# Performance work log

Hardware: AMD Instinct MI355X
Metric: run time of the kernel (lower is better)

The kernel has to match this reference:

```python
import jax, jax.numpy as jnp
import numpy as np

INPUT_DIM = 2048
BATCH = 8192
SCALE = 0.1


def setup_inputs() -> dict:
    key = jax.random.key(0)
    kx, kw, kb = jax.random.split(key, 3)
    x = jax.random.normal(kx, (BATCH, INPUT_DIM), dtype=jnp.float32)
    # torch Linear default init: U(-1/sqrt(fan_in), 1/sqrt(fan_in))
    bound = 1.0 / np.sqrt(INPUT_DIM)
    W = jax.random.uniform(kw, (INPUT_DIM, INPUT_DIM), minval=-bound, maxval=bound, dtype=jnp.float32)
    b = jax.random.uniform(kb, (INPUT_DIM,), minval=-bound, maxval=bound, dtype=jnp.float32)
    return {"x": x, "W": W, "b": b}


def reference(x, W, b):
    # y = fc(x); z = y * scale * scale; out = z.sum(-1)
    y = jnp.einsum('bi,oi->bo', x, W) + b  # Linear stores weight as [out, in]
    z = y * (SCALE * SCALE)
    return z.sum(axis=-1)
```

## Files before the change

kernel.cpp:

```cpp
#include <hip/hip_runtime.h>


constexpr int IN_DIM  = 2048;
constexpr int BATCH   = 8192;
constexpr float SCALE2 = 0.01f;
constexpr int DGROUPS = 8;

__global__ __launch_bounds__(512)
void colsum_partial(const float* __restrict__ W, const float* __restrict__ bias,
                    float* __restrict__ partial, float* __restrict__ bsum) {
    const int t = threadIdx.x;
    const int b = blockIdx.x;
    const int g = b >> 6;
    const int h = b & 63;
    const int lane = t & 63, w = t >> 6;

    const float4* W4 = reinterpret_cast<const float4*>(W);
    const int c4   = (h << 3) + (t & 7);
    const int rsub = t >> 3;
    const size_t base = (size_t)((g << 8) + rsub) * (IN_DIM / 4) + c4;

    float4 acc = {0.f, 0.f, 0.f, 0.f};
    #pragma unroll
    for (int k = 0; k < 4; ++k) {
        const float4 v = W4[base + (size_t)(k << 6) * (IN_DIM / 4)];
        acc.x += v.x; acc.y += v.y; acc.z += v.z; acc.w += v.w;
    }
    #pragma unroll
    for (int m = 8; m <= 32; m <<= 1) {
        acc.x += __shfl_xor(acc.x, m); acc.y += __shfl_xor(acc.y, m);
        acc.z += __shfl_xor(acc.z, m); acc.w += __shfl_xor(acc.w, m);
    }

    __shared__ float4 redA[8][8];
    if (lane < 8) redA[w][lane] = acc;
    __syncthreads();
    if (t < 8) {
        float4 s = redA[0][t];
        #pragma unroll
        for (int j = 1; j < 8; ++j) {
            const float4 v = redA[j][t];
            s.x += v.x; s.y += v.y; s.z += v.z; s.w += v.w;
        }
        reinterpret_cast<float4*>(partial)[(size_t)g * (IN_DIM / 4) + (h << 3) + t] = s;
    }

    if (b == 0) {
        __shared__ float bs_red[8];
        float s = 0.f;
        #pragma unroll
        for (int k = 0; k < 4; ++k) s += bias[t + (k << 9)];
        #pragma unroll
        for (int off = 32; off; off >>= 1) s += __shfl_down(s, off);
        if (lane == 0) bs_red[w] = s;
        __syncthreads();
        if (t == 0) {
            float tot = 0.f;
            #pragma unroll
            for (int j = 0; j < 8; ++j) tot += bs_red[j];
            bsum[0] = tot;
        }
    }
}

__global__ __launch_bounds__(512)
void reduce_matvec(const float* __restrict__ x, const float* __restrict__ partial,
                   const float* __restrict__ bsum, float* __restrict__ out) {
    __shared__ float4 wsh4[IN_DIM / 4];
    __shared__ float  bs_sh;

    const int t    = threadIdx.x;
    const int b    = blockIdx.x;
    const int lane = t & 63;
    const int w    = t >> 6;

    const float4* p4 = reinterpret_cast<const float4*>(partial);
    float4 pv[DGROUPS];
    #pragma unroll
    for (int g = 0; g < DGROUPS; ++g)
        pv[g] = p4[(size_t)g * (IN_DIM / 4) + t];

    const float4* x4 = reinterpret_cast<const float4*>(x);
    const int r0 = (b << 4) + (w << 1);
    const size_t xb = (size_t)r0 * (IN_DIM / 4);
    float4 xv[8];
    #pragma unroll
    for (int k = 0; k < 8; ++k)
        xv[k] = x4[xb + (k << 6) + lane];

    if (t == 0) bs_sh = bsum[0];

    float4 acc = pv[0];
    #pragma unroll
    for (int g = 1; g < DGROUPS; ++g) {
        acc.x += pv[g].x; acc.y += pv[g].y;
        acc.z += pv[g].z; acc.w += pv[g].w;
    }
    wsh4[t] = acc;
    __syncthreads();

    float a0 = 0.f, a1 = 0.f;
    #pragma unroll
    for (int k = 0; k < 8; ++k) {
        const int ci = (k << 6) + lane;
        const float4 wv = wsh4[ci];
        const float4 v1 = x4[xb + 512 + ci];
        a0 += xv[k].x * wv.x + xv[k].y * wv.y + xv[k].z * wv.z + xv[k].w * wv.w;
        a1 += v1.x * wv.x + v1.y * wv.y + v1.z * wv.z + v1.w * wv.w;
    }
    #pragma unroll
    for (int off = 32; off; off >>= 1) {
        a0 += __shfl_down(a0, off);
        a1 += __shfl_down(a1, off);
    }
    if (lane == 0) {
        const float bs = bs_sh;
        *reinterpret_cast<float2*>(out + r0) =
            make_float2(SCALE2 * (a0 + bs), SCALE2 * (a1 + bs));
    }
}

extern "C" void kernel_launch(void* const* d_in, const int* in_sizes, int n_in,
                              void* d_out, int out_size, void* d_ws, size_t ws_size,
                              hipStream_t stream) {
    const float* x    = (const float*)d_in[0];
    const float* W    = (const float*)d_in[1];
    const float* bias = (const float*)d_in[2];
    float* out = (float*)d_out;
    char*  ws  = (char*)d_ws;

    float* partial = (float*)ws;
    float* bsum    = (float*)(ws + (size_t)DGROUPS * IN_DIM * sizeof(float));

    colsum_partial<<<512, 512, 0, stream>>>(W, bias, partial, bsum);
    reduce_matvec<<<BATCH / 16, 512, 0, stream>>>(x, partial, bsum, out);
}
```

Baseline: 21.50 us.

## Fuse column-sum and matvec into one cooperative kernel with grid sync

```diff
diff --git a/kernel.cpp b/kernel.cpp
--- a/kernel.cpp
+++ b/kernel.cpp
@@ -1,10 +1,115 @@
 #include <hip/hip_runtime.h>
+#include <hip/hip_cooperative_groups.h>
+
+namespace cg = cooperative_groups;
 
 
 constexpr int IN_DIM  = 2048;
 constexpr int BATCH   = 8192;
 constexpr float SCALE2 = 0.01f;
 constexpr int DGROUPS = 8;
+constexpr int NBLK    = 256;
+
+__global__ __launch_bounds__(1024, 4)
+void fused(const float* __restrict__ x, const float* __restrict__ W,
+           const float* __restrict__ bias, float* __restrict__ out,
+           float* __restrict__ partial) {
+    const int t    = threadIdx.x;
+    const int b    = blockIdx.x;
+    const int lane = t & 63;
+    const int w    = t >> 6;
+
+    __shared__ float4 wsh4[IN_DIM / 4];
+    __shared__ float4 redA[16][16];
+    __shared__ float  bs_red[16];
+    __shared__ float  bs_sh;
+
+    const float4* W4 = reinterpret_cast<const float4*>(W);
+    const int g    = b >> 5;
+    const int h    = b & 31;
+    const int c4   = (h << 4) + (t & 15);
+    const int rsub = t >> 4;
+    const size_t wbase = (size_t)((g << 8) + rsub) * (IN_DIM / 4) + c4;
+    const float4 wa0 = W4[wbase];
+    const float4 wa1 = W4[wbase + (size_t)64  * (IN_DIM / 4)];
+    const float4 wa2 = W4[wbase + (size_t)128 * (IN_DIM / 4)];
+    const float4 wa3 = W4[wbase + (size_t)192 * (IN_DIM / 4)];
+
+    const float4* x4 = reinterpret_cast<const float4*>(x);
+    const int r0 = (b << 5) + (w << 1);
+    const size_t xb = (size_t)r0 * (IN_DIM / 4);
+    float4 xv[8];
+    #pragma unroll
+    for (int k = 0; k < 8; ++k)
+        xv[k] = x4[xb + (k << 6) + lane];
+
+    float bsv = bias[t] + bias[t + 1024];
+
+    float4 acc = { wa0.x + wa1.x + wa2.x + wa3.x,
+                   wa0.y + wa1.y + wa2.y + wa3.y,
+                   wa0.z + wa1.z + wa2.z + wa3.z,
+                   wa0.w + wa1.w + wa2.w + wa3.w };
+    #pragma unroll
+    for (int m = 16; m <= 32; m <<= 1) {
+        acc.x += __shfl_xor(acc.x, m); acc.y += __shfl_xor(acc.y, m);
+        acc.z += __shfl_xor(acc.z, m); acc.w += __shfl_xor(acc.w, m);
+    }
+    #pragma unroll
+    for (int off = 32; off; off >>= 1) bsv += __shfl_down(bsv, off);
+    if (lane < 16) redA[w][lane] = acc;
+    if (lane == 0) bs_red[w] = bsv;
+    __syncthreads();
+    if (t < 16) {
+        float4 s = redA[0][t];
+        #pragma unroll
+        for (int j = 1; j < 16; ++j) {
+            const float4 v = redA[j][t];
+            s.x += v.x; s.y += v.y; s.z += v.z; s.w += v.w;
+        }
+        reinterpret_cast<float4*>(partial)[(size_t)g * (IN_DIM / 4) + (h << 4) + t] = s;
+    }
+    if (t == 0) {
+        float tot = 0.f;
+        #pragma unroll
+        for (int j = 0; j < 16; ++j) tot += bs_red[j];
+        bs_sh = tot;
+    }
+
+    cg::this_grid().sync();
+
+    if (t < IN_DIM / 4) {
+        const float4* p4 = reinterpret_cast<const float4*>(partial);
+        float4 s = p4[(size_t)(b & (DGROUPS - 1)) * (IN_DIM / 4) + t];
+        #pragma unroll
+        for (int i = 1; i < DGROUPS; ++i) {
+            const int g2 = (i + b) & (DGROUPS - 1);
+            const float4 v = p4[(size_t)g2 * (IN_DIM / 4) + t];
+            s.x += v.x; s.y += v.y; s.z += v.z; s.w += v.w;
+        }
+        wsh4[t] = s;
+    }
+    __syncthreads();
+
+    float a0 = 0.f, a1 = 0.f;
+    #pragma unroll
+    for (int k = 0; k < 8; ++k) {
+        const int ci = (k << 6) + lane;
+        const float4 wv = wsh4[ci];
+        const float4 v1 = x4[xb + 512 + ci];
+        a0 += xv[k].x * wv.x + xv[k].y * wv.y + xv[k].z * wv.z + xv[k].w * wv.w;
+        a1 += v1.x * wv.x + v1.y * wv.y + v1.z * wv.z + v1.w * wv.w;
+    }
+    #pragma unroll
+    for (int off = 32; off; off >>= 1) {
+        a0 += __shfl_down(a0, off);
+        a1 += __shfl_down(a1, off);
+    }
+    if (lane == 0) {
+        const float bs = bs_sh;
+        *reinterpret_cast<float2*>(out + r0) =
+            make_float2(SCALE2 * (a0 + bs), SCALE2 * (a1 + bs));
+    }
+}
 
 __global__ __launch_bounds__(512)
 void colsum_partial(const float* __restrict__ W, const float* __restrict__ bias,
@@ -132,6 +237,22 @@
     float* partial = (float*)ws;
     float* bsum    = (float*)(ws + (size_t)DGROUPS * IN_DIM * sizeof(float));
 
+    int occ = 0;
+    hipError_t qe = hipOccupancyMaxActiveBlocksPerMultiprocessor(
+        &occ, fused, 1024, 0);
+
+    bool coop_ok = (qe == hipSuccess && occ >= 1);
+    if (coop_ok) {
+        const float* xa = x; const float* Wa = W; const float* ba = bias;
+        float* oa = out; float* pa = partial;
+        void* args[] = { (void*)&xa, (void*)&Wa, (void*)&ba,
+                         (void*)&oa, (void*)&pa };
+        hipError_t le = hipLaunchCooperativeKernel(
+            (const void*)fused, dim3(NBLK), dim3(1024), args, 0, stream);
+        if (le == hipSuccess) return;
+        coop_ok = false;
+    }
+
     colsum_partial<<<512, 512, 0, stream>>>(W, bias, partial, bsum);
     reduce_matvec<<<BATCH / 16, 512, 0, stream>>>(x, partial, bsum, out);
 }
```

Result: no change. 21.58 us (+0.4%).

## Process one row per wave in matvec and cut register use for occupancy

Applied to the files above, without the earlier changes.

```diff
diff --git a/kernel.cpp b/kernel.cpp
--- a/kernel.cpp
+++ b/kernel.cpp
@@ -63,7 +63,7 @@
     }
 }
 
-__global__ __launch_bounds__(512)
+__global__ __launch_bounds__(512, 8)
 void reduce_matvec(const float* __restrict__ x, const float* __restrict__ partial,
                    const float* __restrict__ bsum, float* __restrict__ out) {
     __shared__ float4 wsh4[IN_DIM / 4];
@@ -74,15 +74,9 @@
     const int lane = t & 63;
     const int w    = t >> 6;
 
-    const float4* p4 = reinterpret_cast<const float4*>(partial);
-    float4 pv[DGROUPS];
-    #pragma unroll
-    for (int g = 0; g < DGROUPS; ++g)
-        pv[g] = p4[(size_t)g * (IN_DIM / 4) + t];
-
     const float4* x4 = reinterpret_cast<const float4*>(x);
-    const int r0 = (b << 4) + (w << 1);
-    const size_t xb = (size_t)r0 * (IN_DIM / 4);
+    const int row = (b << 3) + w;
+    const size_t xb = (size_t)row * (IN_DIM / 4);
     float4 xv[8];
     #pragma unroll
     for (int k = 0; k < 8; ++k)
@@ -90,34 +84,27 @@
 
     if (t == 0) bs_sh = bsum[0];
 
-    float4 acc = pv[0];
-    #pragma unroll
+    const float4* p4 = reinterpret_cast<const float4*>(partial);
+    float4 s = p4[t];
+    #pragma unroll 2
     for (int g = 1; g < DGROUPS; ++g) {
-        acc.x += pv[g].x; acc.y += pv[g].y;
-        acc.z += pv[g].z; acc.w += pv[g].w;
+        const float4 v = p4[(size_t)g * (IN_DIM / 4) + t];
+        s.x += v.x; s.y += v.y; s.z += v.z; s.w += v.w;
     }
-    wsh4[t] = acc;
+    wsh4[t] = s;
     __syncthreads();
 
-    float a0 = 0.f, a1 = 0.f;
+    float a0 = 0.f;
     #pragma unroll
     for (int k = 0; k < 8; ++k) {
-        const int ci = (k << 6) + lane;
-        const float4 wv = wsh4[ci];
-        const float4 v1 = x4[xb + 512 + ci];
+        const float4 wv = wsh4[(k << 6) + lane];
         a0 += xv[k].x * wv.x + xv[k].y * wv.y + xv[k].z * wv.z + xv[k].w * wv.w;
-        a1 += v1.x * wv.x + v1.y * wv.y + v1.z * wv.z + v1.w * wv.w;
     }
     #pragma unroll
-    for (int off = 32; off; off >>= 1) {
+    for (int off = 32; off; off >>= 1)
         a0 += __shfl_down(a0, off);
-        a1 += __shfl_down(a1, off);
-    }
-    if (lane == 0) {
-        const float bs = bs_sh;
-        *reinterpret_cast<float2*>(out + r0) =
-            make_float2(SCALE2 * (a0 + bs), SCALE2 * (a1 + bs));
-    }
+    if (lane == 0)
+        out[row] = SCALE2 * (a0 + bs_sh);
 }
 
 extern "C" void kernel_launch(void* const* d_in, const int* in_sizes, int n_in,
@@ -133,5 +120,5 @@
     float* bsum    = (float*)(ws + (size_t)DGROUPS * IN_DIM * sizeof(float));
 
     colsum_partial<<<512, 512, 0, stream>>>(W, bias, partial, bsum);
-    reduce_matvec<<<BATCH / 16, 512, 0, stream>>>(x, partial, bsum, out);
+    reduce_matvec<<<BATCH / 8, 512, 0, stream>>>(x, partial, bsum, out);
 }
```

New measurement: 22.13 us. 1.03x slower.
